# Optimization experiments

Hardware: AMD Instinct MI355X
Metric: run time of the kernel (lower is better)

The kernel has to match this reference:

```python
import jax, jax.numpy as jnp
import numpy as np

DIM = 768
NUM_HEADS = 12
DECAY_RATE = 5.0


def setup_inputs() -> dict:
    key = jax.random.key(0)
    k1, k2, k3, k4 = jax.random.split(key, 4)
    B, N, C = 4, 1024, DIM
    x = jax.random.normal(k1, (B, N, C), dtype=jnp.float32)
    # torch nn.Linear weights: y = x @ W.T ; qkv_bias=False
    qkv_w = jax.random.normal(k2, (3 * C, C), dtype=jnp.float32) * (1.0 / np.sqrt(C))
    proj_w = jax.random.normal(k3, (C, C), dtype=jnp.float32) * (1.0 / np.sqrt(C))
    proj_b = jax.random.normal(k4, (C,), dtype=jnp.float32) * 0.01
    return {"x": x, "qkv_w": qkv_w, "proj_w": proj_w, "proj_b": proj_b, "cur_epoch": 3}


def reference(x, qkv_w, proj_w, proj_b, cur_epoch):
    B, N, C = x.shape
    H = NUM_HEADS
    hd = C // H
    scale = hd ** -0.5

    qkv = (x @ qkv_w.T).reshape(B, N, 3, H, hd).transpose(2, 0, 3, 1, 4)  # [3,B,H,N,hd]
    q, k, v = qkv[0], qkv[1], qkv[2]

    scores = jnp.einsum("bhqd,bhkd->bhqk", q, k) * scale
    logp = jax.nn.log_softmax(scores, axis=-1)
    attn = jnp.exp(logp)  # [B,H,N,N]

    # Per-key entropy: column j of attn flattened over (B,H,N) is renormalized
    # by Categorical; dividing by num_heads cancels under normalization.
    # H(p/s) = log(s) - (1/s) * sum(p * log p)
    s = jnp.sum(attn, axis=(0, 1, 2))                 # [N]
    plogp = jnp.sum(attn * logp, axis=(0, 1, 2))      # [N]
    entropies = jnp.log(s) - plogp / s

    # threshold decay: factor = sum_{i=0}^{cur_epoch-1} decay*exp(-(i+1))
    factor = DECAY_RATE * float(np.sum(np.exp(-(np.arange(cur_epoch) + 1.0))))
    entropy_threshold = float(np.log(C)) - factor

    # attn[:,:,:,keep] @ v[:,:,keep,:] == (attn * mask) @ v  (zeroed columns drop out)
    mask = (entropies <= entropy_threshold).astype(attn.dtype)  # [N]
    out = jnp.einsum("bhqk,bhkd->bhqd", attn * mask[None, None, None, :], v)
    out = out.transpose(0, 2, 1, 3).reshape(B, N, C)
    out = out @ proj_w.T + proj_b
    return out
```

## Files before the change

kernel.cpp:

```cpp
#include <hip/hip_runtime.h>


typedef __bf16 bf16x8 __attribute__((ext_vector_type(8)));
typedef __bf16 bf16x4 __attribute__((ext_vector_type(4)));
typedef float  f32x4  __attribute__((ext_vector_type(4)));

#define MFMA16(a, b, c) __builtin_amdgcn_mfma_f32_16x16x32_bf16((a), (b), (c), 0, 0, 0)

__global__ __launch_bounds__(256) void kc_conv(
    const float* __restrict__ x, const float* __restrict__ qw, const float* __restrict__ pw,
    __bf16* __restrict__ xb, __bf16* __restrict__ qwb, __bf16* __restrict__ pwb,
    float* __restrict__ colSP, int* __restrict__ keepCnt)
{
  const int i = blockIdx.x * 256 + threadIdx.x;
  const float4* src;
  __bf16* dst;
  int j;
  if (i < 786432)       { src = (const float4*)x;  dst = xb;  j = i; }
  else if (i < 1228800) { src = (const float4*)qw; dst = qwb; j = i - 786432; }
  else                  { src = (const float4*)pw; dst = pwb; j = i - 1228800; }
  const float4 f = src[j];
  bf16x4 o;
  o[0] = (__bf16)f.x; o[1] = (__bf16)f.y; o[2] = (__bf16)f.z; o[3] = (__bf16)f.w;
  *(bf16x4*)(dst + 4 * (size_t)j) = o;
  if (i < 2048) colSP[i] = 0.f;
  if (i == 0) *keepCnt = 0;
}

__global__ __launch_bounds__(256) void kg_qkv(
    const __bf16* __restrict__ A, const __bf16* __restrict__ Bm,
    __bf16* __restrict__ qb, __bf16* __restrict__ kb, float* __restrict__ v)
{
  __shared__ __bf16 As[64 * 72];
  __shared__ __bf16 Bs[64 * 72];
  const int tid = threadIdx.x;
  const int w = tid >> 6, lane = tid & 63, quad = lane >> 4, l = lane & 15;
  const int r0 = blockIdx.y * 64, c0 = blockIdx.x * 64;
  const int row = tid >> 3, ko = (tid & 7) * 8;
  const f32x4 zero = {0.f, 0.f, 0.f, 0.f};
  f32x4 acc[4];
#pragma unroll
  for (int ct = 0; ct < 4; ++ct) acc[ct] = zero;

  uint4 a0 = *(const uint4*)(A + (size_t)(r0 + row) * 768 + ko);
  uint4 a1 = *(const uint4*)(A + (size_t)(r0 + row + 32) * 768 + ko);
  uint4 b0 = *(const uint4*)(Bm + (size_t)(c0 + row) * 768 + ko);
  uint4 b1 = *(const uint4*)(Bm + (size_t)(c0 + row + 32) * 768 + ko);

  for (int k0 = 0; k0 < 768; k0 += 64) {
    __syncthreads();
    *(uint4*)&As[row * 72 + ko] = a0;
    *(uint4*)&As[(row + 32) * 72 + ko] = a1;
    *(uint4*)&Bs[row * 72 + ko] = b0;
    *(uint4*)&Bs[(row + 32) * 72 + ko] = b1;
    __syncthreads();
    if (k0 < 704) {
      a0 = *(const uint4*)(A + (size_t)(r0 + row) * 768 + k0 + 64 + ko);
      a1 = *(const uint4*)(A + (size_t)(r0 + row + 32) * 768 + k0 + 64 + ko);
      b0 = *(const uint4*)(Bm + (size_t)(c0 + row) * 768 + k0 + 64 + ko);
      b1 = *(const uint4*)(Bm + (size_t)(c0 + row + 32) * 768 + k0 + 64 + ko);
    }
    const bf16x8 af0 = *(const bf16x8*)&As[(w * 16 + l) * 72 + quad * 8];
    const bf16x8 af1 = *(const bf16x8*)&As[(w * 16 + l) * 72 + 32 + quad * 8];
#pragma unroll
    for (int ct = 0; ct < 4; ++ct) {
      const bf16x8 bf0 = *(const bf16x8*)&Bs[(ct * 16 + l) * 72 + quad * 8];
      const bf16x8 bf1 = *(const bf16x8*)&Bs[(ct * 16 + l) * 72 + 32 + quad * 8];
      acc[ct] = MFMA16(af0, bf0, acc[ct]);
      acc[ct] = MFMA16(af1, bf1, acc[ct]);
    }
  }
  const int part = c0 / 768;
  const int h = (c0 % 768) >> 6;
#pragma unroll
  for (int ct = 0; ct < 4; ++ct) {
    const int d = ct * 16 + l;
#pragma unroll
    for (int i = 0; i < 4; ++i) {
      const int rg = r0 + w * 16 + quad * 4 + i;
      const int b_ = rg >> 10, n = rg & 1023;
      const size_t off = ((size_t)(b_ * 12 + h) * 1024 + n) * 64 + d;
      const float val = acc[ct][i];
      if (part == 0)      qb[off] = (__bf16)val;
      else if (part == 1) kb[off] = (__bf16)val;
      else                v[off]  = val;
    }
  }
}

__global__ __launch_bounds__(256) void ks_fused(
    const __bf16* __restrict__ qb, const __bf16* __restrict__ kb,
    float* __restrict__ lse, float* __restrict__ partial)
{
  __shared__ __bf16 Ks[64 * 72];
  __shared__ float sS[1024];
  __shared__ float sP[1024];
  const int tid = threadIdx.x;
  const int w = tid >> 6, lane = tid & 63, quad = lane >> 4, l = lane & 15;
  const int bh = blockIdx.x, r0 = blockIdx.y * 64;
  const int row = tid >> 3, ko = (tid & 7) * 8;
  for (int i = tid; i < 1024; i += 256) { sS[i] = 0.f; sP[i] = 0.f; }

  const __bf16* qrow = qb + ((size_t)bh * 1024 + r0 + w * 16 + l) * 64;
  const bf16x8 aq0 = *(const bf16x8*)(qrow + quad * 8);
  const bf16x8 aq1 = *(const bf16x8*)(qrow + 32 + quad * 8);
  const __bf16* kbase = kb + (size_t)bh * 65536;
  const f32x4 zero = {0.f, 0.f, 0.f, 0.f};

  uint4 ka0 = *(const uint4*)(kbase + (size_t)row * 64 + ko);
  uint4 ka1 = *(const uint4*)(kbase + (size_t)(row + 32) * 64 + ko);

  float z[4] = {0.f, 0.f, 0.f, 0.f};
  for (int chunk = 0; chunk < 16; ++chunk) {
    __syncthreads();
    *(uint4*)&Ks[row * 72 + ko] = ka0;
    *(uint4*)&Ks[(row + 32) * 72 + ko] = ka1;
    __syncthreads();
    const int nxt = (chunk < 15) ? (chunk + 1) : 0;
    ka0 = *(const uint4*)(kbase + (size_t)(nxt * 64 + row) * 64 + ko);
    ka1 = *(const uint4*)(kbase + (size_t)(nxt * 64 + row + 32) * 64 + ko);
#pragma unroll
    for (int ct = 0; ct < 4; ++ct) {
      const bf16x8 kf0 = *(const bf16x8*)&Ks[(ct * 16 + l) * 72 + quad * 8];
      const bf16x8 kf1 = *(const bf16x8*)&Ks[(ct * 16 + l) * 72 + 32 + quad * 8];
      f32x4 acc = MFMA16(aq0, kf0, zero);
      acc = MFMA16(aq1, kf1, acc);
#pragma unroll
      for (int r = 0; r < 4; ++r) z[r] += __expf(acc[r] * 0.125f);
    }
  }
#pragma unroll
  for (int off = 1; off < 16; off <<= 1) {
#pragma unroll
    for (int r = 0; r < 4; ++r) z[r] += __shfl_xor(z[r], off);
  }
  float ls[4];
#pragma unroll
  for (int r = 0; r < 4; ++r) ls[r] = __logf(z[r]);
  if (l == 0) {
#pragma unroll
    for (int r = 0; r < 4; ++r)
      lse[bh * 1024 + r0 + w * 16 + quad * 4 + r] = ls[r];
  }

  for (int chunk = 0; chunk < 16; ++chunk) {
    __syncthreads();
    *(uint4*)&Ks[row * 72 + ko] = ka0;
    *(uint4*)&Ks[(row + 32) * 72 + ko] = ka1;
    __syncthreads();
    if (chunk < 15) {
      ka0 = *(const uint4*)(kbase + (size_t)((chunk + 1) * 64 + row) * 64 + ko);
      ka1 = *(const uint4*)(kbase + (size_t)((chunk + 1) * 64 + row + 32) * 64 + ko);
    }
#pragma unroll
    for (int ct = 0; ct < 4; ++ct) {
      const bf16x8 kf0 = *(const bf16x8*)&Ks[(ct * 16 + l) * 72 + quad * 8];
      const bf16x8 kf1 = *(const bf16x8*)&Ks[(ct * 16 + l) * 72 + 32 + quad * 8];
      f32x4 acc = MFMA16(aq0, kf0, zero);
      acc = MFMA16(aq1, kf1, acc);
      float sp = 0.f, spl = 0.f;
#pragma unroll
      for (int r = 0; r < 4; ++r) {
        const float lp = acc[r] * 0.125f - ls[r];
        const float p = __expf(lp);
        sp += p;
        spl += p * lp;
      }
      sp += __shfl_xor(sp, 16);   sp += __shfl_xor(sp, 32);
      spl += __shfl_xor(spl, 16); spl += __shfl_xor(spl, 32);
      if (lane < 16) {
        atomicAdd(&sS[chunk * 64 + ct * 16 + l], sp);
        atomicAdd(&sP[chunk * 64 + ct * 16 + l], spl);
      }
    }
  }
  __syncthreads();
  float* pb = partial + (size_t)(blockIdx.x * 16 + blockIdx.y) * 2048;
  for (int i = tid; i < 1024; i += 256) {
    pb[i] = sS[i];
    pb[1024 + i] = sP[i];
  }
}

__global__ __launch_bounds__(256) void kr_reduce(
    const float* __restrict__ partial, float* __restrict__ colSP)
{
  const int col = blockIdx.y * 256 + threadIdx.x;
  const float* pb = partial + (size_t)blockIdx.x * 16 * 2048 + col;
  float s = 0.f;
#pragma unroll
  for (int p = 0; p < 16; ++p) s += pb[(size_t)p * 2048];
  atomicAdd(&colSP[col], s);
}

__global__ void k_mask(const float* __restrict__ colSP, const int* __restrict__ cur_epoch,
                       float* __restrict__ mask, int* __restrict__ keepCnt)
{
  const int j = threadIdx.x;
  const float s = colSP[j];
  const float ent = __logf(s) - colSP[1024 + j] / s;
  const int ce = cur_epoch[0];
  float factor = 0.f;
  for (int i = 1; i <= ce; ++i) factor += __expf(-(float)i);
  factor *= 5.0f;
  const float thr = __logf(768.0f) - factor;
  const int keep = (ent <= thr) ? 1 : 0;
  mask[j] = keep ? 1.0f : 0.0f;
  if (keep) atomicAdd(keepCnt, 1);
}

__global__ __launch_bounds__(256) void k_av(
    const __bf16* __restrict__ qb, const __bf16* __restrict__ kb,
    const float* __restrict__ v, const float* __restrict__ lse,
    const float* __restrict__ mask, const int* __restrict__ keepCnt,
    __bf16* __restrict__ ctxb)
{
  if (*keepCnt == 0) return;
  const int tid = threadIdx.x;
  const int bh = blockIdx.x, r0 = blockIdx.y * 32;
  const int b_ = bh / 12, h = bh % 12;
  __shared__ float qs[32][64];
  __shared__ float pbuf[4][8][64];
  for (int i = tid; i < 2048; i += 256)
    qs[i >> 6][i & 63] = (float)qb[((size_t)bh * 1024 + r0) * 64 + i];
  __syncthreads();
  const int w = tid >> 6, l = tid & 63, rb = w * 8;
  float ls[8];
#pragma unroll
  for (int i = 0; i < 8; ++i) ls[i] = lse[bh * 1024 + r0 + rb + i];
  float acc[8] = {};
  for (int chunk = 0; chunk < 16; ++chunk) {
    const float mk = mask[chunk * 64 + l];
    if (__ballot(mk != 0.0f) == 0ull) continue;
    const __bf16* kp = kb + ((size_t)bh * 1024 + chunk * 64 + l) * 64;
    float s[8] = {};
    for (int d0 = 0; d0 < 64; d0 += 8) {
      const bf16x8 kf = *(const bf16x8*)(kp + d0);
#pragma unroll
      for (int dd = 0; dd < 8; ++dd) {
        const float kv = (float)kf[dd];
#pragma unroll
        for (int i = 0; i < 8; ++i) s[i] += qs[rb + i][d0 + dd] * kv;
      }
    }
    __syncthreads();
#pragma unroll
    for (int i = 0; i < 8; ++i)
      pbuf[w][i][l] = __expf(s[i] * 0.125f - ls[i]) * mk;
    __syncthreads();
    const float* vp = v + ((size_t)bh * 1024 + chunk * 64) * 64 + l;
    for (int jj = 0; jj < 64; ++jj) {
      const float vv = vp[(size_t)jj * 64];
#pragma unroll
      for (int i = 0; i < 8; ++i) acc[i] += pbuf[w][i][jj] * vv;
    }
  }
#pragma unroll
  for (int i = 0; i < 8; ++i)
    ctxb[((size_t)(b_ * 1024 + r0 + rb + i)) * 768 + h * 64 + l] = (__bf16)acc[i];
}

__global__ __launch_bounds__(256) void kg_proj(
    const __bf16* __restrict__ A, const __bf16* __restrict__ Bm,
    const float* __restrict__ bias, const int* __restrict__ keepCnt,
    float* __restrict__ out)
{
  const int tid = threadIdx.x;
  const int w = tid >> 6, lane = tid & 63, quad = lane >> 4, l = lane & 15;
  const int r0 = blockIdx.y * 64, c0 = blockIdx.x * 64;
  if (*keepCnt == 0) {
#pragma unroll
    for (int ct = 0; ct < 4; ++ct) {
      const int c = c0 + ct * 16 + l;
      const float bv = bias[c];
#pragma unroll
      for (int i = 0; i < 4; ++i) {
        const int rg = r0 + w * 16 + quad * 4 + i;
        out[(size_t)rg * 768 + c] = bv;
      }
    }
    return;
  }
  __shared__ __bf16 As[64 * 72];
  __shared__ __bf16 Bs[64 * 72];
  const int row = tid >> 3, ko = (tid & 7) * 8;
  const f32x4 zero = {0.f, 0.f, 0.f, 0.f};
  f32x4 acc[4];
#pragma unroll
  for (int ct = 0; ct < 4; ++ct) acc[ct] = zero;

  uint4 a0 = *(const uint4*)(A + (size_t)(r0 + row) * 768 + ko);
  uint4 a1 = *(const uint4*)(A + (size_t)(r0 + row + 32) * 768 + ko);
  uint4 b0 = *(const uint4*)(Bm + (size_t)(c0 + row) * 768 + ko);
  uint4 b1 = *(const uint4*)(Bm + (size_t)(c0 + row + 32) * 768 + ko);

  for (int k0 = 0; k0 < 768; k0 += 64) {
    __syncthreads();
    *(uint4*)&As[row * 72 + ko] = a0;
    *(uint4*)&As[(row + 32) * 72 + ko] = a1;
    *(uint4*)&Bs[row * 72 + ko] = b0;
    *(uint4*)&Bs[(row + 32) * 72 + ko] = b1;
    __syncthreads();
    if (k0 < 704) {
      a0 = *(const uint4*)(A + (size_t)(r0 + row) * 768 + k0 + 64 + ko);
      a1 = *(const uint4*)(A + (size_t)(r0 + row + 32) * 768 + k0 + 64 + ko);
      b0 = *(const uint4*)(Bm + (size_t)(c0 + row) * 768 + k0 + 64 + ko);
      b1 = *(const uint4*)(Bm + (size_t)(c0 + row + 32) * 768 + k0 + 64 + ko);
    }
    const bf16x8 af0 = *(const bf16x8*)&As[(w * 16 + l) * 72 + quad * 8];
    const bf16x8 af1 = *(const bf16x8*)&As[(w * 16 + l) * 72 + 32 + quad * 8];
#pragma unroll
    for (int ct = 0; ct < 4; ++ct) {
      const bf16x8 bf0 = *(const bf16x8*)&Bs[(ct * 16 + l) * 72 + quad * 8];
      const bf16x8 bf1 = *(const bf16x8*)&Bs[(ct * 16 + l) * 72 + 32 + quad * 8];
      acc[ct] = MFMA16(af0, bf0, acc[ct]);
      acc[ct] = MFMA16(af1, bf1, acc[ct]);
    }
  }
#pragma unroll
  for (int ct = 0; ct < 4; ++ct) {
    const int c = c0 + ct * 16 + l;
#pragma unroll
    for (int i = 0; i < 4; ++i) {
      const int rg = r0 + w * 16 + quad * 4 + i;
      out[(size_t)rg * 768 + c] = acc[ct][i] + bias[c];
    }
  }
}

extern "C" void kernel_launch(void* const* d_in, const int* in_sizes, int n_in,
                              void* d_out, int out_size, void* d_ws, size_t ws_size,
                              hipStream_t stream)
{
  const float* x      = (const float*)d_in[0];
  const float* qkv_w  = (const float*)d_in[1];
  const float* proj_w = (const float*)d_in[2];
  const float* proj_b = (const float*)d_in[3];
  const int*   cur_ep = (const int*)d_in[4];

  char* W = (char*)d_ws;
  __bf16* xb    = (__bf16*)(W + 0);
  __bf16* qwb   = (__bf16*)(W + 6291456);
  __bf16* pwb   = (__bf16*)(W + 9830400);
  __bf16* qb    = (__bf16*)(W + 11010048);
  __bf16* kb    = (__bf16*)(W + 17301504);
  float*  v     = (float*) (W + 23592960);
  __bf16* ctxb  = (__bf16*)(W + 36175872);
  float*  lse   = (float*) (W + 42467328);
  float*  mask  = (float*) (W + 42663936);
  int*    keep  = (int*)   (W + 42668032);
  float*  colSP = (float*) (W + 42668544);
  float*  part  = (float*) (W + 42676736);
  float*  out   = (float*)d_out;

  kc_conv<<<5376, 256, 0, stream>>>(x, qkv_w, proj_w, xb, qwb, pwb, colSP, keep);
  kg_qkv<<<dim3(36, 64), 256, 0, stream>>>(xb, qwb, qb, kb, v);
  ks_fused<<<dim3(48, 16), 256, 0, stream>>>(qb, kb, lse, part);
  kr_reduce<<<dim3(48, 8), 256, 0, stream>>>(part, colSP);
  k_mask<<<1, 1024, 0, stream>>>(colSP, cur_ep, mask, keep);
  k_av<<<dim3(48, 32), 256, 0, stream>>>(qb, kb, v, lse, mask, keep, ctxb);
  kg_proj<<<dim3(12, 64), 256, 0, stream>>>(ctxb, pwb, proj_b, keep, out);
}
```

Baseline: 179.9 us.

## Split score kernel column tiles across wave pairs and store partials in bf16

The score/entropy kernel now covers 32 query rows per block instead of 64. Each pair of waves shares a 16-row group and splits the four key column tiles between them, combining row sums through shared memory. This doubles the grid to give more parallelism and less work per wave. Per-block column partials are also written as bf16 instead of fp32 to halve partial traffic, which costs precision in the entropy sums that drive the mask threshold.

```diff
diff --git a/kernel.cpp b/kernel.cpp
--- a/kernel.cpp
+++ b/kernel.cpp
@@ -90,18 +90,21 @@
 
 __global__ __launch_bounds__(256) void ks_fused(
     const __bf16* __restrict__ qb, const __bf16* __restrict__ kb,
-    float* __restrict__ lse, float* __restrict__ partial)
+    float* __restrict__ lse, __bf16* __restrict__ partial)
 {
   __shared__ __bf16 Ks[64 * 72];
   __shared__ float sS[1024];
   __shared__ float sP[1024];
+  __shared__ float zrow[32];
   const int tid = threadIdx.x;
   const int w = tid >> 6, lane = tid & 63, quad = lane >> 4, l = lane & 15;
-  const int bh = blockIdx.x, r0 = blockIdx.y * 64;
+  const int rowg = w >> 1, ctp = (w & 1) * 2;
+  const int bh = blockIdx.x, r0 = blockIdx.y * 32;
   const int row = tid >> 3, ko = (tid & 7) * 8;
   for (int i = tid; i < 1024; i += 256) { sS[i] = 0.f; sP[i] = 0.f; }
-
-  const __bf16* qrow = qb + ((size_t)bh * 1024 + r0 + w * 16 + l) * 64;
+  if (tid < 32) zrow[tid] = 0.f;
+
+  const __bf16* qrow = qb + ((size_t)bh * 1024 + r0 + rowg * 16 + l) * 64;
   const bf16x8 aq0 = *(const bf16x8*)(qrow + quad * 8);
   const bf16x8 aq1 = *(const bf16x8*)(qrow + 32 + quad * 8);
   const __bf16* kbase = kb + (size_t)bh * 65536;
@@ -120,7 +123,8 @@
     ka0 = *(const uint4*)(kbase + (size_t)(nxt * 64 + row) * 64 + ko);
     ka1 = *(const uint4*)(kbase + (size_t)(nxt * 64 + row + 32) * 64 + ko);
 #pragma unroll
-    for (int ct = 0; ct < 4; ++ct) {
+    for (int cc = 0; cc < 2; ++cc) {
+      const int ct = ctp + cc;
       const bf16x8 kf0 = *(const bf16x8*)&Ks[(ct * 16 + l) * 72 + quad * 8];
       const bf16x8 kf1 = *(const bf16x8*)&Ks[(ct * 16 + l) * 72 + 32 + quad * 8];
       f32x4 acc = MFMA16(aq0, kf0, zero);
@@ -134,13 +138,19 @@
 #pragma unroll
     for (int r = 0; r < 4; ++r) z[r] += __shfl_xor(z[r], off);
   }
+  if (l == 0) {
+#pragma unroll
+    for (int r = 0; r < 4; ++r)
+      atomicAdd(&zrow[rowg * 16 + quad * 4 + r], z[r]);
+  }
+  __syncthreads();
   float ls[4];
 #pragma unroll
-  for (int r = 0; r < 4; ++r) ls[r] = __logf(z[r]);
-  if (l == 0) {
+  for (int r = 0; r < 4; ++r) ls[r] = __logf(zrow[rowg * 16 + quad * 4 + r]);
+  if ((w & 1) == 0 && l == 0) {
 #pragma unroll
     for (int r = 0; r < 4; ++r)
-      lse[bh * 1024 + r0 + w * 16 + quad * 4 + r] = ls[r];
+      lse[bh * 1024 + r0 + rowg * 16 + quad * 4 + r] = ls[r];
   }
 
   for (int chunk = 0; chunk < 16; ++chunk) {
@@ -153,7 +163,8 @@
       ka1 = *(const uint4*)(kbase + (size_t)((chunk + 1) * 64 + row + 32) * 64 + ko);
     }
 #pragma unroll
-    for (int ct = 0; ct < 4; ++ct) {
+    for (int cc = 0; cc < 2; ++cc) {
+      const int ct = ctp + cc;
       const bf16x8 kf0 = *(const bf16x8*)&Ks[(ct * 16 + l) * 72 + quad * 8];
       const bf16x8 kf1 = *(const bf16x8*)&Ks[(ct * 16 + l) * 72 + 32 + quad * 8];
       f32x4 acc = MFMA16(aq0, kf0, zero);
@@ -175,21 +186,21 @@
     }
   }
   __syncthreads();
-  float* pb = partial + (size_t)(blockIdx.x * 16 + blockIdx.y) * 2048;
+  __bf16* pb = partial + (size_t)(blockIdx.x * 32 + blockIdx.y) * 2048;
   for (int i = tid; i < 1024; i += 256) {
-    pb[i] = sS[i];
-    pb[1024 + i] = sP[i];
+    pb[i] = (__bf16)sS[i];
+    pb[1024 + i] = (__bf16)sP[i];
   }
 }
 
 __global__ __launch_bounds__(256) void kr_reduce(
-    const float* __restrict__ partial, float* __restrict__ colSP)
+    const __bf16* __restrict__ partial, float* __restrict__ colSP)
 {
   const int col = blockIdx.y * 256 + threadIdx.x;
-  const float* pb = partial + (size_t)blockIdx.x * 16 * 2048 + col;
+  const __bf16* pb = partial + (size_t)blockIdx.x * 16 * 2048 + col;
   float s = 0.f;
 #pragma unroll
-  for (int p = 0; p < 16; ++p) s += pb[(size_t)p * 2048];
+  for (int p = 0; p < 16; ++p) s += (float)pb[(size_t)p * 2048];
   atomicAdd(&colSP[col], s);
 }
 
@@ -350,13 +361,13 @@
   float*  mask  = (float*) (W + 42663936);
   int*    keep  = (int*)   (W + 42668032);
   float*  colSP = (float*) (W + 42668544);
-  float*  part  = (float*) (W + 42676736);
+  __bf16* part  = (__bf16*)(W + 42676736);
   float*  out   = (float*)d_out;
 
   kc_conv<<<5376, 256, 0, stream>>>(x, qkv_w, proj_w, xb, qwb, pwb, colSP, keep);
   kg_qkv<<<dim3(36, 64), 256, 0, stream>>>(xb, qwb, qb, kb, v);
-  ks_fused<<<dim3(48, 16), 256, 0, stream>>>(qb, kb, lse, part);
-  kr_reduce<<<dim3(48, 8), 256, 0, stream>>>(part, colSP);
+  ks_fused<<<dim3(48, 32), 256, 0, stream>>>(qb, kb, lse, part);
+  kr_reduce<<<dim3(96, 8), 256, 0, stream>>>(part, colSP);
   k_mask<<<1, 1024, 0, stream>>>(colSP, cur_ep, mask, keep);
   k_av<<<dim3(48, 32), 256, 0, stream>>>(qb, kb, v, lse, mask, keep, ctxb);
   kg_proj<<<dim3(12, 64), 256, 0, stream>>>(ctxb, pwb, proj_b, keep, out);
```

Result: slower. 185.3 us (+3.0%).

## Split softmax stats into row-sum and column-stats kernels with key-parallel MFMA

Applied to the files above, without the earlier changes.

Replaces the fused two-pass score kernel and its partial-sum reduction with three kernels. One computes row partition sums with atomics over split key halves, one turns them into lse and 1/Z terms, and one computes column entropy sums with each wave owning key columns and streaming queries. The column stats are rewritten algebraically as p·lp = e/Z·s − e·logZ/Z, which removes the LDS staging, syncs, shared atomics and the partial buffer. The cost is recomputing QK^T twice from global/L2 loads without LDS reuse, plus global atomics and extra launches.

```diff
diff --git a/kernel.cpp b/kernel.cpp
--- a/kernel.cpp
+++ b/kernel.cpp
@@ -6,11 +6,12 @@
 typedef float  f32x4  __attribute__((ext_vector_type(4)));
 
 #define MFMA16(a, b, c) __builtin_amdgcn_mfma_f32_16x16x32_bf16((a), (b), (c), 0, 0, 0)
+#define LOG2E_8 0.18033688f
 
 __global__ __launch_bounds__(256) void kc_conv(
     const float* __restrict__ x, const float* __restrict__ qw, const float* __restrict__ pw,
     __bf16* __restrict__ xb, __bf16* __restrict__ qwb, __bf16* __restrict__ pwb,
-    float* __restrict__ colSP, int* __restrict__ keepCnt)
+    float* __restrict__ colSP, float* __restrict__ rowZ, int* __restrict__ keepCnt)
 {
   const int i = blockIdx.x * 256 + threadIdx.x;
   const float4* src;
@@ -24,6 +25,7 @@
   o[0] = (__bf16)f.x; o[1] = (__bf16)f.y; o[2] = (__bf16)f.z; o[3] = (__bf16)f.w;
   *(bf16x4*)(dst + 4 * (size_t)j) = o;
   if (i < 2048) colSP[i] = 0.f;
+  if (i < 49152) rowZ[i] = 0.f;
   if (i == 0) *keepCnt = 0;
 }
 
@@ -88,109 +90,93 @@
   }
 }
 
-__global__ __launch_bounds__(256) void ks_fused(
+__global__ __launch_bounds__(256) void k_rowz(
     const __bf16* __restrict__ qb, const __bf16* __restrict__ kb,
-    float* __restrict__ lse, float* __restrict__ partial)
-{
-  __shared__ __bf16 Ks[64 * 72];
-  __shared__ float sS[1024];
-  __shared__ float sP[1024];
+    float* __restrict__ rowZ)
+{
   const int tid = threadIdx.x;
   const int w = tid >> 6, lane = tid & 63, quad = lane >> 4, l = lane & 15;
-  const int bh = blockIdx.x, r0 = blockIdx.y * 64;
-  const int row = tid >> 3, ko = (tid & 7) * 8;
-  for (int i = tid; i < 1024; i += 256) { sS[i] = 0.f; sP[i] = 0.f; }
-
+  const int bh = blockIdx.x, r0 = blockIdx.y * 64, cbase = blockIdx.z * 512;
   const __bf16* qrow = qb + ((size_t)bh * 1024 + r0 + w * 16 + l) * 64;
   const bf16x8 aq0 = *(const bf16x8*)(qrow + quad * 8);
   const bf16x8 aq1 = *(const bf16x8*)(qrow + 32 + quad * 8);
-  const __bf16* kbase = kb + (size_t)bh * 65536;
+  const __bf16* kbase = kb + ((size_t)bh * 1024 + cbase + l) * 64 + quad * 8;
   const f32x4 zero = {0.f, 0.f, 0.f, 0.f};
-
-  uint4 ka0 = *(const uint4*)(kbase + (size_t)row * 64 + ko);
-  uint4 ka1 = *(const uint4*)(kbase + (size_t)(row + 32) * 64 + ko);
-
   float z[4] = {0.f, 0.f, 0.f, 0.f};
-  for (int chunk = 0; chunk < 16; ++chunk) {
-    __syncthreads();
-    *(uint4*)&Ks[row * 72 + ko] = ka0;
-    *(uint4*)&Ks[(row + 32) * 72 + ko] = ka1;
-    __syncthreads();
-    const int nxt = (chunk < 15) ? (chunk + 1) : 0;
-    ka0 = *(const uint4*)(kbase + (size_t)(nxt * 64 + row) * 64 + ko);
-    ka1 = *(const uint4*)(kbase + (size_t)(nxt * 64 + row + 32) * 64 + ko);
-#pragma unroll
-    for (int ct = 0; ct < 4; ++ct) {
-      const bf16x8 kf0 = *(const bf16x8*)&Ks[(ct * 16 + l) * 72 + quad * 8];
-      const bf16x8 kf1 = *(const bf16x8*)&Ks[(ct * 16 + l) * 72 + 32 + quad * 8];
-      f32x4 acc = MFMA16(aq0, kf0, zero);
-      acc = MFMA16(aq1, kf1, acc);
-#pragma unroll
-      for (int r = 0; r < 4; ++r) z[r] += __expf(acc[r] * 0.125f);
-    }
+#pragma unroll 8
+  for (int chunk = 0; chunk < 32; ++chunk) {
+    const __bf16* kp = kbase + (size_t)chunk * 16 * 64;
+    const bf16x8 kf0 = *(const bf16x8*)kp;
+    const bf16x8 kf1 = *(const bf16x8*)(kp + 32);
+    f32x4 acc = MFMA16(aq0, kf0, zero);
+    acc = MFMA16(aq1, kf1, acc);
+#pragma unroll
+    for (int r = 0; r < 4; ++r) z[r] += exp2f(acc[r] * LOG2E_8);
   }
 #pragma unroll
   for (int off = 1; off < 16; off <<= 1) {
 #pragma unroll
     for (int r = 0; r < 4; ++r) z[r] += __shfl_xor(z[r], off);
   }
-  float ls[4];
-#pragma unroll
-  for (int r = 0; r < 4; ++r) ls[r] = __logf(z[r]);
   if (l == 0) {
 #pragma unroll
     for (int r = 0; r < 4; ++r)
-      lse[bh * 1024 + r0 + w * 16 + quad * 4 + r] = ls[r];
-  }
-
-  for (int chunk = 0; chunk < 16; ++chunk) {
-    __syncthreads();
-    *(uint4*)&Ks[row * 72 + ko] = ka0;
-    *(uint4*)&Ks[(row + 32) * 72 + ko] = ka1;
-    __syncthreads();
-    if (chunk < 15) {
-      ka0 = *(const uint4*)(kbase + (size_t)((chunk + 1) * 64 + row) * 64 + ko);
-      ka1 = *(const uint4*)(kbase + (size_t)((chunk + 1) * 64 + row + 32) * 64 + ko);
-    }
-#pragma unroll
-    for (int ct = 0; ct < 4; ++ct) {
-      const bf16x8 kf0 = *(const bf16x8*)&Ks[(ct * 16 + l) * 72 + quad * 8];
-      const bf16x8 kf1 = *(const bf16x8*)&Ks[(ct * 16 + l) * 72 + 32 + quad * 8];
-      f32x4 acc = MFMA16(aq0, kf0, zero);
-      acc = MFMA16(aq1, kf1, acc);
-      float sp = 0.f, spl = 0.f;
-#pragma unroll
-      for (int r = 0; r < 4; ++r) {
-        const float lp = acc[r] * 0.125f - ls[r];
-        const float p = __expf(lp);
-        sp += p;
-        spl += p * lp;
-      }
-      sp += __shfl_xor(sp, 16);   sp += __shfl_xor(sp, 32);
-      spl += __shfl_xor(spl, 16); spl += __shfl_xor(spl, 32);
-      if (lane < 16) {
-        atomicAdd(&sS[chunk * 64 + ct * 16 + l], sp);
-        atomicAdd(&sP[chunk * 64 + ct * 16 + l], spl);
-      }
-    }
-  }
-  __syncthreads();
-  float* pb = partial + (size_t)(blockIdx.x * 16 + blockIdx.y) * 2048;
-  for (int i = tid; i < 1024; i += 256) {
-    pb[i] = sS[i];
-    pb[1024 + i] = sP[i];
-  }
-}
-
-__global__ __launch_bounds__(256) void kr_reduce(
-    const float* __restrict__ partial, float* __restrict__ colSP)
-{
-  const int col = blockIdx.y * 256 + threadIdx.x;
-  const float* pb = partial + (size_t)blockIdx.x * 16 * 2048 + col;
-  float s = 0.f;
-#pragma unroll
-  for (int p = 0; p < 16; ++p) s += pb[(size_t)p * 2048];
-  atomicAdd(&colSP[col], s);
+      atomicAdd(&rowZ[bh * 1024 + r0 + w * 16 + quad * 4 + r], z[r]);
+  }
+}
+
+__global__ void k_lsefin(const float* __restrict__ rowZ, float* __restrict__ lse,
+                         float* __restrict__ uw)
+{
+  const int i = blockIdx.x * 256 + threadIdx.x;
+  const float Z = rowZ[i];
+  const float lg = __logf(Z);
+  const float u = 1.0f / Z;
+  lse[i] = lg;
+  float2 p; p.x = u; p.y = lg * u;
+  *(float2*)(uw + 2 * (size_t)i) = p;
+}
+
+__global__ __launch_bounds__(256) void k_colstats(
+    const __bf16* __restrict__ qb, const __bf16* __restrict__ kb,
+    const float* __restrict__ uw, float* __restrict__ colSP)
+{
+  const int tid = threadIdx.x;
+  const int w = tid >> 6, lane = tid & 63, quad = lane >> 4, l = lane & 15;
+  const int bh = blockIdx.x, c0 = blockIdx.y * 64, mbase = blockIdx.z * 512;
+  const __bf16* krow = kb + ((size_t)bh * 1024 + c0 + w * 16 + l) * 64;
+  const bf16x8 kf0 = *(const bf16x8*)(krow + quad * 8);
+  const bf16x8 kf1 = *(const bf16x8*)(krow + 32 + quad * 8);
+  const __bf16* qbase = qb + ((size_t)bh * 1024 + mbase + l) * 64 + quad * 8;
+  const float* uwbase = uw + 2 * ((size_t)bh * 1024 + mbase + quad * 4);
+  const f32x4 zero = {0.f, 0.f, 0.f, 0.f};
+  float cs = 0.f, cp = 0.f;
+#pragma unroll 8
+  for (int chunk = 0; chunk < 32; ++chunk) {
+    const __bf16* qp = qbase + (size_t)chunk * 16 * 64;
+    const bf16x8 aq0 = *(const bf16x8*)qp;
+    const bf16x8 aq1 = *(const bf16x8*)(qp + 32);
+    const float4 uw0 = *(const float4*)(uwbase + chunk * 32);
+    const float4 uw1 = *(const float4*)(uwbase + chunk * 32 + 4);
+    f32x4 acc = MFMA16(aq0, kf0, zero);
+    acc = MFMA16(aq1, kf1, acc);
+    const float uu[4] = {uw0.x, uw0.z, uw1.x, uw1.z};
+    const float ww[4] = {uw0.y, uw0.w, uw1.y, uw1.w};
+#pragma unroll
+    for (int r = 0; r < 4; ++r) {
+      const float sg = acc[r] * 0.125f;
+      const float e = exp2f(acc[r] * LOG2E_8);
+      const float t = e * uu[r];
+      cs += t;
+      cp += t * sg - e * ww[r];
+    }
+  }
+  cs += __shfl_xor(cs, 16); cs += __shfl_xor(cs, 32);
+  cp += __shfl_xor(cp, 16); cp += __shfl_xor(cp, 32);
+  if (lane < 16) {
+    atomicAdd(&colSP[c0 + w * 16 + l], cs);
+    atomicAdd(&colSP[1024 + c0 + w * 16 + l], cp);
+  }
 }
 
 __global__ void k_mask(const float* __restrict__ colSP, const int* __restrict__ cur_epoch,
@@ -350,13 +336,15 @@
   float*  mask  = (float*) (W + 42663936);
   int*    keep  = (int*)   (W + 42668032);
   float*  colSP = (float*) (W + 42668544);
-  float*  part  = (float*) (W + 42676736);
+  float*  rowZ  = (float*) (W + 42676736);
+  float*  uw    = (float*) (W + 42873344);
   float*  out   = (float*)d_out;
 
-  kc_conv<<<5376, 256, 0, stream>>>(x, qkv_w, proj_w, xb, qwb, pwb, colSP, keep);
+  kc_conv<<<5376, 256, 0, stream>>>(x, qkv_w, proj_w, xb, qwb, pwb, colSP, rowZ, keep);
   kg_qkv<<<dim3(36, 64), 256, 0, stream>>>(xb, qwb, qb, kb, v);
-  ks_fused<<<dim3(48, 16), 256, 0, stream>>>(qb, kb, lse, part);
-  kr_reduce<<<dim3(48, 8), 256, 0, stream>>>(part, colSP);
+  k_rowz<<<dim3(48, 16, 2), 256, 0, stream>>>(qb, kb, rowZ);
+  k_lsefin<<<192, 256, 0, stream>>>(rowZ, lse, uw);
+  k_colstats<<<dim3(48, 16, 2), 256, 0, stream>>>(qb, kb, uw, colSP);
   k_mask<<<1, 1024, 0, stream>>>(colSP, cur_ep, mask, keep);
   k_av<<<dim3(48, 32), 256, 0, stream>>>(qb, kb, v, lse, mask, keep, ctxb);
   kg_proj<<<dim3(12, 64), 256, 0, stream>>>(ctxb, pwb, proj_b, keep, out);
```

Result: slower. 225.0 us (+25.1%).

## Enlarge K staging tiles, use exp2 math, fold partial reduction into atomics

Applied to the files above, without the earlier changes.

The score/entropy kernel now stages 256 keys per shared-memory tile instead of 64, cutting the number of barrier-separated stages from 16 to 4 per pass. Exponentials use exp2f with a pre-folded log2e scale, and the p·log p term is rewritten algebraically so that no per-element subtraction of the log-sum-exp is needed. The separate partial-sum reduction kernel and its scratch buffer are removed; each block atomically adds its column sums straight into the global accumulator. This trades one launch and a global round-trip for more shared memory (lower occupancy), more registers for prefetch, and heavier global atomic contention.

```diff
diff --git a/kernel.cpp b/kernel.cpp
--- a/kernel.cpp
+++ b/kernel.cpp
@@ -6,6 +6,7 @@
 typedef float  f32x4  __attribute__((ext_vector_type(4)));
 
 #define MFMA16(a, b, c) __builtin_amdgcn_mfma_f32_16x16x32_bf16((a), (b), (c), 0, 0, 0)
+#define LOG2E_8 0.18033688f
 
 __global__ __launch_bounds__(256) void kc_conv(
     const float* __restrict__ x, const float* __restrict__ qw, const float* __restrict__ pw,
@@ -90,43 +91,46 @@
 
 __global__ __launch_bounds__(256) void ks_fused(
     const __bf16* __restrict__ qb, const __bf16* __restrict__ kb,
-    float* __restrict__ lse, float* __restrict__ partial)
-{
-  __shared__ __bf16 Ks[64 * 72];
+    float* __restrict__ lse, float* __restrict__ colSP)
+{
+  __shared__ __bf16 Ks[256 * 72];
   __shared__ float sS[1024];
   __shared__ float sP[1024];
   const int tid = threadIdx.x;
   const int w = tid >> 6, lane = tid & 63, quad = lane >> 4, l = lane & 15;
   const int bh = blockIdx.x, r0 = blockIdx.y * 64;
-  const int row = tid >> 3, ko = (tid & 7) * 8;
   for (int i = tid; i < 1024; i += 256) { sS[i] = 0.f; sP[i] = 0.f; }
 
   const __bf16* qrow = qb + ((size_t)bh * 1024 + r0 + w * 16 + l) * 64;
   const bf16x8 aq0 = *(const bf16x8*)(qrow + quad * 8);
   const bf16x8 aq1 = *(const bf16x8*)(qrow + 32 + quad * 8);
-  const __bf16* kbase = kb + (size_t)bh * 65536;
+  const uint4* kb4 = (const uint4*)(kb + (size_t)bh * 65536);
   const f32x4 zero = {0.f, 0.f, 0.f, 0.f};
 
-  uint4 ka0 = *(const uint4*)(kbase + (size_t)row * 64 + ko);
-  uint4 ka1 = *(const uint4*)(kbase + (size_t)(row + 32) * 64 + ko);
+  uint4 kreg[8];
+#pragma unroll
+  for (int i = 0; i < 8; ++i) kreg[i] = kb4[i * 256 + tid];
 
   float z[4] = {0.f, 0.f, 0.f, 0.f};
-  for (int chunk = 0; chunk < 16; ++chunk) {
-    __syncthreads();
-    *(uint4*)&Ks[row * 72 + ko] = ka0;
-    *(uint4*)&Ks[(row + 32) * 72 + ko] = ka1;
-    __syncthreads();
-    const int nxt = (chunk < 15) ? (chunk + 1) : 0;
-    ka0 = *(const uint4*)(kbase + (size_t)(nxt * 64 + row) * 64 + ko);
-    ka1 = *(const uint4*)(kbase + (size_t)(nxt * 64 + row + 32) * 64 + ko);
-#pragma unroll
-    for (int ct = 0; ct < 4; ++ct) {
+  for (int stage = 0; stage < 4; ++stage) {
+    __syncthreads();
+#pragma unroll
+    for (int i = 0; i < 8; ++i) {
+      const int g = i * 256 + tid;
+      *(uint4*)&Ks[(g >> 3) * 72 + (g & 7) * 8] = kreg[i];
+    }
+    __syncthreads();
+    const int nxt = (stage < 3) ? (stage + 1) : 0;
+#pragma unroll
+    for (int i = 0; i < 8; ++i) kreg[i] = kb4[nxt * 2048 + i * 256 + tid];
+#pragma unroll
+    for (int ct = 0; ct < 16; ++ct) {
       const bf16x8 kf0 = *(const bf16x8*)&Ks[(ct * 16 + l) * 72 + quad * 8];
       const bf16x8 kf1 = *(const bf16x8*)&Ks[(ct * 16 + l) * 72 + 32 + quad * 8];
       f32x4 acc = MFMA16(aq0, kf0, zero);
       acc = MFMA16(aq1, kf1, acc);
 #pragma unroll
-      for (int r = 0; r < 4; ++r) z[r] += __expf(acc[r] * 0.125f);
+      for (int r = 0; r < 4; ++r) z[r] += exp2f(acc[r] * LOG2E_8);
     }
   }
 #pragma unroll
@@ -134,63 +138,55 @@
 #pragma unroll
     for (int r = 0; r < 4; ++r) z[r] += __shfl_xor(z[r], off);
   }
-  float ls[4];
-#pragma unroll
-  for (int r = 0; r < 4; ++r) ls[r] = __logf(z[r]);
-  if (l == 0) {
-#pragma unroll
-    for (int r = 0; r < 4; ++r)
-      lse[bh * 1024 + r0 + w * 16 + quad * 4 + r] = ls[r];
-  }
-
-  for (int chunk = 0; chunk < 16; ++chunk) {
-    __syncthreads();
-    *(uint4*)&Ks[row * 72 + ko] = ka0;
-    *(uint4*)&Ks[(row + 32) * 72 + ko] = ka1;
-    __syncthreads();
-    if (chunk < 15) {
-      ka0 = *(const uint4*)(kbase + (size_t)((chunk + 1) * 64 + row) * 64 + ko);
-      ka1 = *(const uint4*)(kbase + (size_t)((chunk + 1) * 64 + row + 32) * 64 + ko);
-    }
-#pragma unroll
-    for (int ct = 0; ct < 4; ++ct) {
+  float uu[4], ww[4];
+#pragma unroll
+  for (int r = 0; r < 4; ++r) {
+    const float lg = __logf(z[r]);
+    uu[r] = 1.0f / z[r];
+    ww[r] = lg * uu[r];
+    if (l == 0) lse[bh * 1024 + r0 + w * 16 + quad * 4 + r] = lg;
+  }
+
+  for (int stage = 0; stage < 4; ++stage) {
+    __syncthreads();
+#pragma unroll
+    for (int i = 0; i < 8; ++i) {
+      const int g = i * 256 + tid;
+      *(uint4*)&Ks[(g >> 3) * 72 + (g & 7) * 8] = kreg[i];
+    }
+    __syncthreads();
+    if (stage < 3) {
+#pragma unroll
+      for (int i = 0; i < 8; ++i) kreg[i] = kb4[(stage + 1) * 2048 + i * 256 + tid];
+    }
+#pragma unroll
+    for (int ct = 0; ct < 16; ++ct) {
       const bf16x8 kf0 = *(const bf16x8*)&Ks[(ct * 16 + l) * 72 + quad * 8];
       const bf16x8 kf1 = *(const bf16x8*)&Ks[(ct * 16 + l) * 72 + 32 + quad * 8];
       f32x4 acc = MFMA16(aq0, kf0, zero);
       acc = MFMA16(aq1, kf1, acc);
-      float sp = 0.f, spl = 0.f;
+      float cs = 0.f, cp = 0.f;
 #pragma unroll
       for (int r = 0; r < 4; ++r) {
-        const float lp = acc[r] * 0.125f - ls[r];
-        const float p = __expf(lp);
-        sp += p;
-        spl += p * lp;
+        const float sg = acc[r] * 0.125f;
+        const float e = exp2f(acc[r] * LOG2E_8);
+        const float t = e * uu[r];
+        cs += t;
+        cp += t * sg - e * ww[r];
       }
-      sp += __shfl_xor(sp, 16);   sp += __shfl_xor(sp, 32);
-      spl += __shfl_xor(spl, 16); spl += __shfl_xor(spl, 32);
+      cs += __shfl_xor(cs, 16); cs += __shfl_xor(cs, 32);
+      cp += __shfl_xor(cp, 16); cp += __shfl_xor(cp, 32);
       if (lane < 16) {
-        atomicAdd(&sS[chunk * 64 + ct * 16 + l], sp);
-        atomicAdd(&sP[chunk * 64 + ct * 16 + l], spl);
+        atomicAdd(&sS[stage * 256 + ct * 16 + l], cs);
+        atomicAdd(&sP[stage * 256 + ct * 16 + l], cp);
       }
     }
   }
   __syncthreads();
-  float* pb = partial + (size_t)(blockIdx.x * 16 + blockIdx.y) * 2048;
   for (int i = tid; i < 1024; i += 256) {
-    pb[i] = sS[i];
-    pb[1024 + i] = sP[i];
-  }
-}
-
-__global__ __launch_bounds__(256) void kr_reduce(
-    const float* __restrict__ partial, float* __restrict__ colSP)
-{
-  const int col = blockIdx.y * 256 + threadIdx.x;
-  const float* pb = partial + (size_t)blockIdx.x * 16 * 2048 + col;
-  float s = 0.f;
-#pragma unroll
-  for (int p = 0; p < 16; ++p) s += pb[(size_t)p * 2048];
-  atomicAdd(&colSP[col], s);
+    atomicAdd(&colSP[i], sS[i]);
+    atomicAdd(&colSP[1024 + i], sP[i]);
+  }
 }
 
 __global__ void k_mask(const float* __restrict__ colSP, const int* __restrict__ cur_epoch,
@@ -350,13 +346,11 @@
   float*  mask  = (float*) (W + 42663936);
   int*    keep  = (int*)   (W + 42668032);
   float*  colSP = (float*) (W + 42668544);
-  float*  part  = (float*) (W + 42676736);
   float*  out   = (float*)d_out;
 
   kc_conv<<<5376, 256, 0, stream>>>(x, qkv_w, proj_w, xb, qwb, pwb, colSP, keep);
   kg_qkv<<<dim3(36, 64), 256, 0, stream>>>(xb, qwb, qb, kb, v);
-  ks_fused<<<dim3(48, 16), 256, 0, stream>>>(qb, kb, lse, part);
-  kr_reduce<<<dim3(48, 8), 256, 0, stream>>>(part, colSP);
+  ks_fused<<<dim3(48, 16), 256, 0, stream>>>(qb, kb, lse, colSP);
   k_mask<<<1, 1024, 0, stream>>>(colSP, cur_ep, mask, keep);
   k_av<<<dim3(48, 32), 256, 0, stream>>>(qb, kb, v, lse, mask, keep, ctxb);
   kg_proj<<<dim3(12, 64), 256, 0, stream>>>(ctxb, pwb, proj_b, keep, out);
```

Result: slower. 213.6 us (+18.7%).
